# Kernel tuning notes

Measured on AMD Instinct MI355X. Metric: run time of the kernel, lower is better.

## Reference

```python
import jax, jax.numpy as jnp
import numpy as np

B, T, L = 4, 256, 216
E_PC, E_ROOT, E_QUAL = 12, 12, 16
W_NM = 0.1    # pc_non_matching_score_weight
W_ADV = 0.001 # adversarial_score_weight


def _seg_mean(x):
    # x: [B,T,E] -> mean over frames s..e (inclusive) for all (s,e): [B,T_s,T_e,E]
    # computed with a prefix sum instead of the O(T^2) python loop of the source
    b, t, e = x.shape
    cs = jnp.concatenate([jnp.zeros((b, 1, e), x.dtype), jnp.cumsum(x, axis=1)], axis=1)
    seg_sum = cs[:, None, 1:, :] - cs[:, :-1, None, :]  # cs[e+1] - cs[s]
    idx = jnp.arange(t)
    len_c = jnp.maximum(idx[None, :] - idx[:, None] + 1, 1).astype(x.dtype)  # e-s+1, clipped
    return seg_sum / len_c[None, :, :, None]


def setup_inputs() -> dict:
    key = jax.random.key(0)
    ks = jax.random.split(key, 9)
    return {
        "active_pc": jax.random.uniform(ks[0], (B, T, E_PC), jnp.float32),
        "active_root": jax.random.uniform(ks[1], (B, T, E_ROOT), jnp.float32),
        "active_quality": jax.random.uniform(ks[2], (B, T, E_QUAL), jnp.float32),
        "inactive_pc": jax.random.uniform(ks[3], (B, T, E_PC), jnp.float32),
        "inactive_root": jax.random.uniform(ks[4], (B, T, E_ROOT), jnp.float32),
        "inactive_quality": jax.random.uniform(ks[5], (B, T, E_QUAL), jnp.float32),
        "harmony_pc": jax.random.uniform(ks[6], (B, L, E_PC), jnp.float32),
        "harmony_root": jax.random.uniform(ks[7], (B, L, E_ROOT), jnp.float32),
        "harmony_quality": jax.random.uniform(ks[8], (B, L, E_QUAL), jnp.float32),
        "pc_only": 0,
    }


def reference(active_pc, active_root, active_quality,
              inactive_pc, inactive_root, inactive_quality,
              harmony_pc, harmony_root, harmony_quality, pc_only):
    idx = jnp.arange(T)
    valid = idx[None, :] >= idx[:, None]  # end >= start

    Hs = harmony_pc.sum(-1)               # [B,L]
    Mpc = _seg_mean(active_pc)            # [B,T,T,E_PC]
    A = jnp.einsum('bste,ble->bstl', Mpc, harmony_pc)  # [B,T,T,L]

    # pc matching + adversarial terms (source uses active_pc for the 'inactive'
    # pc segment; faithful). Algebraically fused:
    #   A - W_NM*(MpcSum - A) - W_NM*(Hs - A) - W_ADV*A/Hs
    score = A * ((1.0 + 2.0 * W_NM) - W_ADV / Hs[:, None, None, :]) \
            - W_NM * (Mpc.sum(-1)[..., None] + Hs[:, None, None, :])

    if not pc_only:
        for act, inact, Hc in ((active_root, inactive_root, harmony_root),
                               (active_quality, inactive_quality, harmony_quality)):
            # mean(act)@Hc^T - W_ADV * mean(inact)@Hc^T, fused into one einsum
            Mcomb = _seg_mean(act) - W_ADV * _seg_mean(inact)
            score = score + jnp.einsum('bstd,bld->bstl', Mcomb, Hc)

    return jnp.where(valid[None, :, :, None], score, jnp.zeros((), score.dtype))
```

## Files before the change

### kernel.cpp

```cpp
#include <hip/hip_runtime.h>


typedef float f32x4 __attribute__((ext_vector_type(4)));

#define TT 256
#define LL 216
#define E_PC 12
#define E_ROOT 12
#define E_QUAL 16
#define KK 42
#define CS_STRIDE 44
#define W_NM_C 0.1f
#define W_ADV_C 0.001f

#define ETILE 64
#define NT 256

#define CS_FLOATS (4 * 257 * CS_STRIDE)
#define HM_FLOATS (4 * KK * LL)

__global__ void prep_kernel(const float* __restrict__ apc,
                            const float* __restrict__ aroot,
                            const float* __restrict__ aqual,
                            const float* __restrict__ iroot,
                            const float* __restrict__ iqual,
                            const float* __restrict__ hpc,
                            const float* __restrict__ hroot,
                            const float* __restrict__ hqual,
                            float* __restrict__ CS,
                            float* __restrict__ HM) {
    int blk = blockIdx.x;
    int tid = threadIdx.x;
    if (blk < 4) {
        int b = blk;
        float* cs = CS + b * 257 * CS_STRIDE;
        int k = tid;
        if (k < 40) {
            float acc = 0.f;
            cs[k] = 0.f;
            if (k < 12) {
                const float* p = apc + (size_t)(b * TT) * E_PC + k;
                for (int t = 0; t < TT; ++t) {
                    acc += p[t * E_PC];
                    cs[(t + 1) * CS_STRIDE + k] = acc;
                }
            } else if (k < 24) {
                const float* pa = aroot + (size_t)(b * TT) * E_ROOT + (k - 12);
                const float* pi = iroot + (size_t)(b * TT) * E_ROOT + (k - 12);
                for (int t = 0; t < TT; ++t) {
                    acc += pa[t * E_ROOT] - W_ADV_C * pi[t * E_ROOT];
                    cs[(t + 1) * CS_STRIDE + k] = acc;
                }
            } else {
                const float* pa = aqual + (size_t)(b * TT) * E_QUAL + (k - 24);
                const float* pi = iqual + (size_t)(b * TT) * E_QUAL + (k - 24);
                for (int t = 0; t < TT; ++t) {
                    acc += pa[t * E_QUAL] - W_ADV_C * pi[t * E_QUAL];
                    cs[(t + 1) * CS_STRIDE + k] = acc;
                }
            }
        }
        __syncthreads();
        for (int t = tid; t < 257; t += blockDim.x) {
            float s = 0.f;
            #pragma unroll
            for (int j = 0; j < 12; ++j) s += cs[t * CS_STRIDE + j];
            cs[t * CS_STRIDE + 40] = s;
        }
    } else {
        int b = blk - 4;
        int l = tid;
        if (l < LL) {
            const float* hp = hpc + (size_t)(b * LL + l) * E_PC;
            float hs = 0.f;
            #pragma unroll
            for (int j = 0; j < 12; ++j) hs += hp[j];
            float f = (1.0f + 2.0f * W_NM_C) - W_ADV_C / hs;
            float* hm = HM + (size_t)b * KK * LL + l;
            #pragma unroll
            for (int j = 0; j < 12; ++j) hm[j * LL] = hp[j] * f;
            const float* hr = hroot + (size_t)(b * LL + l) * E_ROOT;
            #pragma unroll
            for (int j = 0; j < 12; ++j) hm[(12 + j) * LL] = hr[j];
            const float* hq = hqual + (size_t)(b * LL + l) * E_QUAL;
            #pragma unroll
            for (int j = 0; j < 16; ++j) hm[(24 + j) * LL] = hq[j];
            hm[40 * LL] = -W_NM_C;
            hm[41 * LL] = -W_NM_C * hs;
        }
    }
}

__global__ __launch_bounds__(NT) void seg_score_kernel(
        const float* __restrict__ CS,
        const float* __restrict__ HM,
        float* __restrict__ out) {
    const int et_blk = blockIdx.x;
    const int s = blockIdx.y;
    const int b = blockIdx.z;
    const int e0 = et_blk * ETILE;
    const int tid = threadIdx.x;

    float* outp = out + ((size_t)(b * TT + s)) * TT * LL + (size_t)e0 * LL;

    if (e0 + ETILE - 1 < s) {
        const f32x4 z = {0.f, 0.f, 0.f, 0.f};
        for (int i = tid; i < (ETILE * LL) / 4; i += NT)
            __builtin_nontemporal_store(z, ((f32x4*)outp) + i);
        return;
    }

    __shared__ float M[KK][ETILE];

    const float* cs = CS + (size_t)b * 257 * CS_STRIDE;

    for (int idx = tid; idx < KK * ETILE; idx += NT) {
        int k = idx >> 6;
        int e = idx & 63;
        int eg = e0 + e;
        float v;
        if (k == 41) {
            v = 1.0f;
        } else {
            int len = eg - s + 1;
            if (len < 1) len = 1;
            v = (cs[(eg + 1) * CS_STRIDE + k] - cs[s * CS_STRIDE + k]) / (float)len;
        }
        M[k][e] = v;
    }
    __syncthreads();

    if (tid < 216) {
        const int lt = tid % 27;
        const int et = tid / 27;
        const int eb = et * 8;
        const int lA = lt * 4;
        const int lB = 108 + lt * 4;

        const float* hA = HM + (size_t)b * KK * LL + lA;
        const float* hB = HM + (size_t)b * KK * LL + lB;

        float acc[8][8];
        #pragma unroll
        for (int i = 0; i < 8; ++i)
            #pragma unroll
            for (int j = 0; j < 8; ++j) acc[i][j] = 0.f;

        #pragma unroll 6
        for (int k = 0; k < KK; ++k) {
            const f32x4 m0 = *(const f32x4*)&M[k][eb];
            const f32x4 m1 = *(const f32x4*)&M[k][eb + 4];
            const f32x4 h0 = *(const f32x4*)(hA + (size_t)k * LL);
            const f32x4 h1 = *(const f32x4*)(hB + (size_t)k * LL);
            const float mv[8] = {m0[0], m0[1], m0[2], m0[3],
                                 m1[0], m1[1], m1[2], m1[3]};
            const float hv[8] = {h0[0], h0[1], h0[2], h0[3],
                                 h1[0], h1[1], h1[2], h1[3]};
            #pragma unroll
            for (int i = 0; i < 8; ++i)
                #pragma unroll
                for (int j = 0; j < 8; ++j)
                    acc[i][j] = fmaf(mv[i], hv[j], acc[i][j]);
        }

        #pragma unroll
        for (int i = 0; i < 8; ++i) {
            const int eg = e0 + eb + i;
            const bool valid = (eg >= s);
            f32x4 v0, v1;
            v0[0] = valid ? acc[i][0] : 0.f;
            v0[1] = valid ? acc[i][1] : 0.f;
            v0[2] = valid ? acc[i][2] : 0.f;
            v0[3] = valid ? acc[i][3] : 0.f;
            v1[0] = valid ? acc[i][4] : 0.f;
            v1[1] = valid ? acc[i][5] : 0.f;
            v1[2] = valid ? acc[i][6] : 0.f;
            v1[3] = valid ? acc[i][7] : 0.f;
            float* row = outp + (size_t)(eb + i) * LL;
            __builtin_nontemporal_store(v0, (f32x4*)(row + lA));
            __builtin_nontemporal_store(v1, (f32x4*)(row + lB));
        }
    }
}

extern "C" void kernel_launch(void* const* d_in, const int* in_sizes, int n_in,
                              void* d_out, int out_size, void* d_ws, size_t ws_size,
                              hipStream_t stream) {
    const float* apc   = (const float*)d_in[0];
    const float* aroot = (const float*)d_in[1];
    const float* aqual = (const float*)d_in[2];
    const float* iroot = (const float*)d_in[4];
    const float* iqual = (const float*)d_in[5];
    const float* hpc   = (const float*)d_in[6];
    const float* hroot = (const float*)d_in[7];
    const float* hqual = (const float*)d_in[8];

    float* CS = (float*)d_ws;
    float* HM = CS + CS_FLOATS;
    float* outp = (float*)d_out;

    prep_kernel<<<8, 256, 0, stream>>>(apc, aroot, aqual, iroot, iqual,
                                       hpc, hroot, hqual, CS, HM);
    seg_score_kernel<<<dim3(4, 256, 4), NT, 0, stream>>>(CS, HM, outp);
}
```

Measured before the change: 339.5 us.

## Process two start rows per block, stage harmony in LDS, peel rank-1 terms

After: 316.0 us. 1.07x faster.

```diff
diff --git a/kernel.cpp b/kernel.cpp
--- a/kernel.cpp
+++ b/kernel.cpp
@@ -8,16 +8,17 @@
 #define E_PC 12
 #define E_ROOT 12
 #define E_QUAL 16
-#define KK 42
+#define KR 40
+#define KM 41
 #define CS_STRIDE 44
 #define W_NM_C 0.1f
 #define W_ADV_C 0.001f
 
 #define ETILE 64
-#define NT 256
+#define NT 512
 
 #define CS_FLOATS (4 * 257 * CS_STRIDE)
-#define HM_FLOATS (4 * KK * LL)
+#define HM_FLOATS (4 * KM * LL)
 
 __global__ void prep_kernel(const float* __restrict__ apc,
                             const float* __restrict__ aroot,
@@ -76,7 +77,7 @@
             #pragma unroll
             for (int j = 0; j < 12; ++j) hs += hp[j];
             float f = (1.0f + 2.0f * W_NM_C) - W_ADV_C / hs;
-            float* hm = HM + (size_t)b * KK * LL + l;
+            float* hm = HM + (size_t)b * KM * LL + l;
             #pragma unroll
             for (int j = 0; j < 12; ++j) hm[j * LL] = hp[j] * f;
             const float* hr = hroot + (size_t)(b * LL + l) * E_ROOT;
@@ -85,73 +86,83 @@
             const float* hq = hqual + (size_t)(b * LL + l) * E_QUAL;
             #pragma unroll
             for (int j = 0; j < 16; ++j) hm[(24 + j) * LL] = hq[j];
-            hm[40 * LL] = -W_NM_C;
-            hm[41 * LL] = -W_NM_C * hs;
+            hm[40 * LL] = -W_NM_C * hs;
         }
     }
 }
 
-__global__ __launch_bounds__(NT) void seg_score_kernel(
+__global__ __launch_bounds__(NT, 4) void seg_score_kernel(
         const float* __restrict__ CS,
         const float* __restrict__ HM,
         float* __restrict__ out) {
     const int et_blk = blockIdx.x;
-    const int s = blockIdx.y;
+    const int sy = blockIdx.y;
     const int b = blockIdx.z;
     const int e0 = et_blk * ETILE;
+    const int s0 = sy * 2;
     const int tid = threadIdx.x;
 
-    float* outp = out + ((size_t)(b * TT + s)) * TT * LL + (size_t)e0 * LL;
-
-    if (e0 + ETILE - 1 < s) {
+    float* outp = out + ((size_t)(b * TT + s0)) * TT * LL + (size_t)e0 * LL;
+
+    if (e0 + ETILE - 1 < s0) {
         const f32x4 z = {0.f, 0.f, 0.f, 0.f};
-        for (int i = tid; i < (ETILE * LL) / 4; i += NT)
-            __builtin_nontemporal_store(z, ((f32x4*)outp) + i);
+        f32x4* o0 = (f32x4*)outp;
+        f32x4* o1 = (f32x4*)(outp + (size_t)TT * LL);
+        for (int i = tid; i < (ETILE * LL) / 4; i += NT) {
+            o0[i] = z;
+            o1[i] = z;
+        }
         return;
     }
 
-    __shared__ float M[KK][ETILE];
+    __shared__ float M[2][KM][ETILE];
+    __shared__ __align__(16) float H[KM][LL];
 
     const float* cs = CS + (size_t)b * 257 * CS_STRIDE;
 
-    for (int idx = tid; idx < KK * ETILE; idx += NT) {
-        int k = idx >> 6;
+    for (int idx = tid; idx < 2 * KM * ETILE; idx += NT) {
+        int h = idx / (KM * ETILE);
+        int r = idx - h * (KM * ETILE);
+        int k = r >> 6;
         int e = idx & 63;
+        int sv = s0 + h;
         int eg = e0 + e;
-        float v;
-        if (k == 41) {
-            v = 1.0f;
-        } else {
-            int len = eg - s + 1;
-            if (len < 1) len = 1;
-            v = (cs[(eg + 1) * CS_STRIDE + k] - cs[s * CS_STRIDE + k]) / (float)len;
-        }
-        M[k][e] = v;
+        int len = eg - sv + 1;
+        if (len < 1) len = 1;
+        M[h][k][e] = (cs[(eg + 1) * CS_STRIDE + k] - cs[sv * CS_STRIDE + k])
+                     / (float)len;
+    }
+    {
+        const f32x4* src = (const f32x4*)(HM + (size_t)b * KM * LL);
+        f32x4* dst = (f32x4*)&H[0][0];
+        for (int i = tid; i < (KM * LL) / 4; i += NT)
+            dst[i] = src[i];
     }
     __syncthreads();
 
-    if (tid < 216) {
-        const int lt = tid % 27;
-        const int et = tid / 27;
+    const int half = tid >> 8;
+    const int t = tid & 255;
+    const int s = s0 + half;
+
+    if (t < 216) {
+        const int lt = t % 27;
+        const int et = t / 27;
         const int eb = et * 8;
         const int lA = lt * 4;
         const int lB = 108 + lt * 4;
 
-        const float* hA = HM + (size_t)b * KK * LL + lA;
-        const float* hB = HM + (size_t)b * KK * LL + lB;
-
         float acc[8][8];
         #pragma unroll
         for (int i = 0; i < 8; ++i)
             #pragma unroll
             for (int j = 0; j < 8; ++j) acc[i][j] = 0.f;
 
-        #pragma unroll 6
-        for (int k = 0; k < KK; ++k) {
-            const f32x4 m0 = *(const f32x4*)&M[k][eb];
-            const f32x4 m1 = *(const f32x4*)&M[k][eb + 4];
-            const f32x4 h0 = *(const f32x4*)(hA + (size_t)k * LL);
-            const f32x4 h1 = *(const f32x4*)(hB + (size_t)k * LL);
+        #pragma unroll 4
+        for (int k = 0; k < KR; ++k) {
+            const f32x4 m0 = *(const f32x4*)&M[half][k][eb];
+            const f32x4 m1 = *(const f32x4*)&M[half][k][eb + 4];
+            const f32x4 h0 = *(const f32x4*)&H[k][lA];
+            const f32x4 h1 = *(const f32x4*)&H[k][lB];
             const float mv[8] = {m0[0], m0[1], m0[2], m0[3],
                                  m1[0], m1[1], m1[2], m1[3]};
             const float hv[8] = {h0[0], h0[1], h0[2], h0[3],
@@ -163,22 +174,28 @@
                     acc[i][j] = fmaf(mv[i], hv[j], acc[i][j]);
         }
 
+        float ex_e[8];
+        #pragma unroll
+        for (int i = 0; i < 8; ++i) ex_e[i] = -W_NM_C * M[half][40][eb + i];
+        const f32x4 xl0 = *(const f32x4*)&H[40][lA];
+        const f32x4 xl1 = *(const f32x4*)&H[40][lB];
+        const float ex_l[8] = {xl0[0], xl0[1], xl0[2], xl0[3],
+                               xl1[0], xl1[1], xl1[2], xl1[3]};
+
+        float* outh = outp + (size_t)half * TT * LL;
         #pragma unroll
         for (int i = 0; i < 8; ++i) {
             const int eg = e0 + eb + i;
             const bool valid = (eg >= s);
             f32x4 v0, v1;
-            v0[0] = valid ? acc[i][0] : 0.f;
-            v0[1] = valid ? acc[i][1] : 0.f;
-            v0[2] = valid ? acc[i][2] : 0.f;
-            v0[3] = valid ? acc[i][3] : 0.f;
-            v1[0] = valid ? acc[i][4] : 0.f;
-            v1[1] = valid ? acc[i][5] : 0.f;
-            v1[2] = valid ? acc[i][6] : 0.f;
-            v1[3] = valid ? acc[i][7] : 0.f;
-            float* row = outp + (size_t)(eb + i) * LL;
-            __builtin_nontemporal_store(v0, (f32x4*)(row + lA));
-            __builtin_nontemporal_store(v1, (f32x4*)(row + lB));
+            #pragma unroll
+            for (int j = 0; j < 4; ++j) {
+                v0[j] = valid ? (acc[i][j] + ex_e[i] + ex_l[j]) : 0.f;
+                v1[j] = valid ? (acc[i][j + 4] + ex_e[i] + ex_l[j + 4]) : 0.f;
+            }
+            float* row = outh + (size_t)(eb + i) * LL;
+            *(f32x4*)(row + lA) = v0;
+            *(f32x4*)(row + lB) = v1;
         }
     }
 }
@@ -201,5 +218,5 @@
 
     prep_kernel<<<8, 256, 0, stream>>>(apc, aroot, aqual, iroot, iqual,
                                        hpc, hroot, hqual, CS, HM);
-    seg_score_kernel<<<dim3(4, 256, 4), NT, 0, stream>>>(CS, HM, outp);
+    seg_score_kernel<<<dim3(4, 128, 4), NT, 0, stream>>>(CS, HM, outp);
 }
```
